# Kernel optimization log

Measured on AMD Instinct MI355X. Metric: run time of the kernel, lower is better.

The kernel has to match this reference:

```python
import jax, jax.numpy as jnp
import numpy as np

HIDDEN = 2048
N_HEADS = 32
N_KV = 8
HEAD_DIM = 128
EPS = 1e-6
THETA = 10000.0
WINDOW = 512
T = 2048


def _rms_norm(x, w, eps=EPS):
    # x: [..., d]
    var = jnp.mean(x * x, axis=-1, keepdims=True)
    return x * jax.lax.rsqrt(var + eps) * w


def _rope(x, positions):
    # neox-style full rotary, x: [T, H, d]
    d = x.shape[-1]
    inv_freq = 1.0 / (THETA ** (jnp.arange(0, d, 2, dtype=jnp.float32) / d))  # [d/2]
    ang = positions.astype(jnp.float32)[:, None] * inv_freq  # [T, d/2]
    cos = jnp.cos(ang)[:, None, :]  # [T,1,d/2]
    sin = jnp.sin(ang)[:, None, :]
    x1, x2 = x[..., : d // 2], x[..., d // 2 :]
    return jnp.concatenate([x1 * cos - x2 * sin, x2 * cos + x1 * sin], axis=-1)


def setup_inputs() -> dict:
    key = jax.random.key(0)
    ks = jax.random.split(key, 6)
    q_size = N_HEADS * HEAD_DIM
    kv_size = N_KV * HEAD_DIM
    s = 1.0 / np.sqrt(HIDDEN)
    return {
        "positions": jnp.arange(T, dtype=jnp.int32),
        "hidden_states": jax.random.normal(ks[0], (T, HIDDEN), dtype=jnp.float32),
        "w_qkv": jax.random.normal(ks[1], (HIDDEN, q_size + 2 * kv_size), dtype=jnp.float32) * s,
        "w_o": jax.random.normal(ks[2], (q_size, HIDDEN), dtype=jnp.float32) * s,
        "w_g": jax.random.normal(ks[3], (HIDDEN, N_HEADS), dtype=jnp.float32) * s,
        "q_norm_w": jnp.ones((HEAD_DIM,), dtype=jnp.float32),
        "k_norm_w": jnp.ones((HEAD_DIM,), dtype=jnp.float32),
    }


def reference(positions, hidden_states, w_qkv, w_o, w_g, q_norm_w, k_norm_w):
    t = hidden_states.shape[0]
    q_size = N_HEADS * HEAD_DIM
    kv_size = N_KV * HEAD_DIM
    scale = HEAD_DIM ** -0.5
    group = N_HEADS // N_KV

    qkv = hidden_states @ w_qkv  # [T, q+2kv]
    q = qkv[:, :q_size].reshape(t, N_HEADS, HEAD_DIM)
    k = qkv[:, q_size : q_size + kv_size].reshape(t, N_KV, HEAD_DIM)
    v = qkv[:, q_size + kv_size :].reshape(t, N_KV, HEAD_DIM)

    # per-head RMSNorm then RoPE
    q = _rope(_rms_norm(q, q_norm_w), positions)
    k = _rope(_rms_norm(k, k_norm_w), positions)

    # sliding-window causal attention with GQA (group queries per kv head)
    qg = q.reshape(t, N_KV, group, HEAD_DIM)
    scores = jnp.einsum("tkgd,skd->kgts", qg, k) * scale  # [Hkv,G,T,T]
    diff = positions[:, None] - positions[None, :]  # i - j
    mask = (diff >= 0) & (diff < WINDOW)  # causal + sliding window
    scores = jnp.where(mask[None, None], scores, -jnp.inf)
    probs = jax.nn.softmax(scores, axis=-1)
    attn = jnp.einsum("kgts,skd->tkgd", probs, v).reshape(t, N_HEADS, HEAD_DIM)

    # softplus gate per head, then output projection
    gate = jax.nn.softplus((hidden_states @ w_g).astype(jnp.float32)).astype(attn.dtype)
    attn = attn * gate[:, :, None]
    return attn.reshape(t, q_size) @ w_o
```

## Files before the change

### kernel.cpp

```cpp
#include <hip/hip_runtime.h>

typedef __attribute__((ext_vector_type(4))) float floatx4;
typedef __attribute__((ext_vector_type(8))) _Float16 half8;
typedef __attribute__((ext_vector_type(4))) _Float16 half4;

#define TT 2048
#define HIDDEN 2048
#define NH 32
#define NKV 8
#define HD 128
#define QSIZE 4096
#define KVSIZE 1024
#define QKVN 6144
#define QKVNP 6272
#define VOFF 5120
#define GOFF 6144
#define WINDOW 512

__global__ __launch_bounds__(256) void prep_kernel(
    const float* __restrict__ w_qkv, const float* __restrict__ w_o,
    const float* __restrict__ hidden, _Float16* __restrict__ Wqkvt,
    _Float16* __restrict__ Wot, _Float16* __restrict__ Xb) {
  __shared__ float tile[64][68];
  int bid = blockIdx.x;
  int tid = threadIdx.x;
  if (bid >= 5120) {
    if (bid < 7168) {
      int i = ((bid - 5120) * 256 + tid) * 8;
      float4 a = *(const float4*)&hidden[i];
      float4 b = *(const float4*)&hidden[i + 4];
      alignas(16) _Float16 o[8] = {(_Float16)a.x, (_Float16)a.y, (_Float16)a.z, (_Float16)a.w,
                                   (_Float16)b.x, (_Float16)b.y, (_Float16)b.z, (_Float16)b.w};
      *(uint4*)&Xb[i] = *(const uint4*)o;
    } else {
      int i = ((bid - 7168) * 256 + tid) * 8;
      *(uint4*)&Wqkvt[(size_t)(GOFF + NH) * HIDDEN + i] = (uint4){0, 0, 0, 0};
    }
    return;
  }
  const float* in;
  _Float16* out;
  int R, C, tilesX, t;
  if (bid < 3072) { in = w_qkv; out = Wqkvt; R = HIDDEN; C = QKVN; tilesX = 96; t = bid; }
  else           { in = w_o;   out = Wot;   R = QSIZE;  C = HIDDEN; tilesX = 32; t = bid - 3072; }
  int bc = (t % tilesX) * 64, br = (t / tilesX) * 64;
  int rr = tid >> 4, l16 = tid & 15;
#pragma unroll
  for (int it = 0; it < 4; ++it) {
    int r = rr + it * 16;
    *(float4*)&tile[r][l16 * 4] = *(const float4*)&in[(size_t)(br + r) * C + bc + l16 * 4];
  }
  __syncthreads();
  int orow = tid >> 2, rr0 = (tid & 3) * 16;
  alignas(16) _Float16 tmp[16];
#pragma unroll
  for (int jj = 0; jj < 16; ++jj) tmp[jj] = (_Float16)tile[rr0 + jj][orow];
  *(uint4*)&out[(size_t)(bc + orow) * R + br + rr0] = *(const uint4*)&tmp[0];
  *(uint4*)&out[(size_t)(bc + orow) * R + br + rr0 + 8] = *(const uint4*)&tmp[8];
}

__global__ __launch_bounds__(256) void transpose_f32_f16_kernel(
    const float* __restrict__ in, _Float16* __restrict__ out, int R, int C) {
  __shared__ float tile[32][33];
  int bc = blockIdx.x * 32;
  int br = blockIdx.y * 32;
  int c = threadIdx.x & 31;
  int r0 = threadIdx.x >> 5;
#pragma unroll
  for (int i = 0; i < 4; ++i) {
    int r = r0 + 8 * i;
    tile[r][c] = in[(size_t)(br + r) * C + bc + c];
  }
  __syncthreads();
#pragma unroll
  for (int i = 0; i < 4; ++i) {
    int r = r0 + 8 * i;
    out[(size_t)(bc + r) * R + br + c] = (_Float16)tile[c][r];
  }
}

__global__ __launch_bounds__(256) void repack_kv_kernel(const _Float16* __restrict__ Kh,
                                                        const _Float16* __restrict__ QKVh,
                                                        _Float16* __restrict__ Kf,
                                                        _Float16* __restrict__ Vf) {
  __shared__ _Float16 tile[64][136];
  int st = blockIdx.x, kh = blockIdx.y;
  int s0 = st * 64;
  if (blockIdx.z == 0) {
    _Float16* dst = Kf + (size_t)(kh * 32 + st) * 8192;
#pragma unroll
    for (int i = 0; i < 4; ++i) {
      int c = threadIdx.x + i * 256;
      int jt = c >> 8, kc = (c >> 6) & 3, quad = (c >> 4) & 3, n16 = c & 15;
      uint4 v = *(const uint4*)&Kh[((size_t)(s0 + jt * 16 + n16) * NKV + kh) * HD +
                                   kc * 32 + quad * 8];
      *(uint4*)&dst[c * 8] = v;
    }
  } else {
#pragma unroll
    for (int i = 0; i < 4; ++i) {
      int c = threadIdx.x + i * 256;
      int row = c >> 4, part = c & 15;
      *(uint4*)&tile[row][part * 8] =
          *(const uint4*)&QKVh[(size_t)(s0 + row) * QKVNP + VOFF + kh * HD + part * 8];
    }
    __syncthreads();
    _Float16* dst = Vf + (size_t)(kh * 32 + st) * 8192;
#pragma unroll
    for (int i = 0; i < 4; ++i) {
      int c = threadIdx.x + i * 256;
      int jd = c >> 7, kc = (c >> 6) & 1, quad = (c >> 4) & 3, n16 = c & 15;
      int d = jd * 16 + n16, sb = kc * 32 + quad * 8;
      alignas(16) _Float16 tmp[8];
#pragma unroll
      for (int j = 0; j < 8; ++j) tmp[j] = tile[sb + j][d];
      *(uint4*)&dst[c * 8] = *(const uint4*)tmp;
    }
  }
}

__device__ __forceinline__ void async16(const _Float16* g, _Float16* l) {
  __builtin_amdgcn_global_load_lds((const __attribute__((address_space(1))) void*)g,
                                   (__attribute__((address_space(3))) void*)l, 16, 0, 0);
}

__device__ __forceinline__ void swizzle_mn(int& m0, int& n0) {
  int ntiles = gridDim.y;
  int pid = blockIdx.x + blockIdx.y * gridDim.x;
  int band = pid / (8 * ntiles);
  int wi = pid - band * (8 * ntiles);
  m0 = (band * 8 + (wi & 7)) * 128;
  n0 = (wi >> 3) * 128;
}

template <typename OutT>
__global__ __launch_bounds__(256, 2) void gemm_bt_kernel(
    const _Float16* __restrict__ A, const _Float16* __restrict__ Bt,
    OutT* __restrict__ C, int M, int N, int K) {
  __shared__ _Float16 As[128 * 64];
  __shared__ _Float16 Bs[128 * 64];
  int tid = threadIdx.x;
  int wave = tid >> 6, lane = tid & 63;
  int wm = wave >> 1, wn = wave & 1;
  int m0, n0;
  swizzle_mn(m0, n0);
  int lr = lane & 15;
  int quad = lane >> 4;
  floatx4 acc[4][4];
#pragma unroll
  for (int i = 0; i < 4; ++i)
#pragma unroll
    for (int j = 0; j < 4; ++j) acc[i][j] = (floatx4){0.f, 0.f, 0.f, 0.f};

  for (int k0 = 0; k0 < K; k0 += 64) {
    __syncthreads();
#pragma unroll
    for (int it = 0; it < 4; ++it) {
      int c = tid + it * 256;
      int row = c >> 3, j = c & 7;
      int jj = j ^ (row & 7);
      _Float16* la = &As[it * 2048 + wave * 512];
      _Float16* lb = &Bs[it * 2048 + wave * 512];
      async16(&A[(size_t)(m0 + row) * K + k0 + jj * 8], la);
      async16(&Bt[(size_t)(n0 + row) * K + k0 + jj * 8], lb);
    }
    __syncthreads();
#pragma unroll
    for (int kc = 0; kc < 2; ++kc) {
      int ch = kc * 4 + quad;
      half8 a[4], b[4];
#pragma unroll
      for (int i = 0; i < 4; ++i) {
        int r = wm * 64 + i * 16 + lr;
        a[i] = *(const half8*)&As[r * 64 + (ch ^ (r & 7)) * 8];
      }
#pragma unroll
      for (int j = 0; j < 4; ++j) {
        int r = wn * 64 + j * 16 + lr;
        b[j] = *(const half8*)&Bs[r * 64 + (ch ^ (r & 7)) * 8];
      }
#pragma unroll
      for (int i = 0; i < 4; ++i)
#pragma unroll
        for (int j = 0; j < 4; ++j)
          acc[i][j] = __builtin_amdgcn_mfma_f32_16x16x32_f16(a[i], b[j], acc[i][j], 0, 0, 0);
    }
  }
  int rq = quad * 4;
#pragma unroll
  for (int i = 0; i < 4; ++i)
#pragma unroll
    for (int j = 0; j < 4; ++j)
#pragma unroll
      for (int r = 0; r < 4; ++r) {
        int row = m0 + wm * 64 + i * 16 + rq + r;
        int col = n0 + wn * 64 + j * 16 + lr;
        C[(size_t)row * N + col] = (OutT)acc[i][j][r];
      }
}

__global__ __launch_bounds__(256, 2) void gemm_bt_splitk_kernel(
    const _Float16* __restrict__ A, const _Float16* __restrict__ Bt,
    float* __restrict__ C, int M, int N, int K, int Ks) {
  __shared__ _Float16 As[128 * 64];
  __shared__ _Float16 Bs[128 * 64];
  int tid = threadIdx.x;
  int wave = tid >> 6, lane = tid & 63;
  int wm = wave >> 1, wn = wave & 1;
  int m0, n0;
  swizzle_mn(m0, n0);
  int kb = blockIdx.z * Ks;
  int lr = lane & 15;
  int quad = lane >> 4;
  floatx4 acc[4][4];
#pragma unroll
  for (int i = 0; i < 4; ++i)
#pragma unroll
    for (int j = 0; j < 4; ++j) acc[i][j] = (floatx4){0.f, 0.f, 0.f, 0.f};

  for (int k0 = kb; k0 < kb + Ks; k0 += 64) {
    __syncthreads();
#pragma unroll
    for (int it = 0; it < 4; ++it) {
      int c = tid + it * 256;
      int row = c >> 3, j = c & 7;
      int jj = j ^ (row & 7);
      _Float16* la = &As[it * 2048 + wave * 512];
      _Float16* lb = &Bs[it * 2048 + wave * 512];
      async16(&A[(size_t)(m0 + row) * K + k0 + jj * 8], la);
      async16(&Bt[(size_t)(n0 + row) * K + k0 + jj * 8], lb);
    }
    __syncthreads();
#pragma unroll
    for (int kc = 0; kc < 2; ++kc) {
      int ch = kc * 4 + quad;
      half8 a[4], b[4];
#pragma unroll
      for (int i = 0; i < 4; ++i) {
        int r = wm * 64 + i * 16 + lr;
        a[i] = *(const half8*)&As[r * 64 + (ch ^ (r & 7)) * 8];
      }
#pragma unroll
      for (int j = 0; j < 4; ++j) {
        int r = wn * 64 + j * 16 + lr;
        b[j] = *(const half8*)&Bs[r * 64 + (ch ^ (r & 7)) * 8];
      }
#pragma unroll
      for (int i = 0; i < 4; ++i)
#pragma unroll
        for (int j = 0; j < 4; ++j)
          acc[i][j] = __builtin_amdgcn_mfma_f32_16x16x32_f16(a[i], b[j], acc[i][j], 0, 0, 0);
    }
  }
  int rq = quad * 4;
#pragma unroll
  for (int i = 0; i < 4; ++i)
#pragma unroll
    for (int j = 0; j < 4; ++j)
#pragma unroll
      for (int r = 0; r < 4; ++r) {
        int row = m0 + wm * 64 + i * 16 + rq + r;
        int col = n0 + wn * 64 + j * 16 + lr;
        unsafeAtomicAdd(&C[(size_t)row * N + col], acc[i][j][r]);
      }
}

__global__ __launch_bounds__(256) void normrope_kernel(
    const _Float16* __restrict__ qkv, const float* __restrict__ qw,
    const float* __restrict__ kw, const int* __restrict__ positions,
    _Float16* __restrict__ qh, _Float16* __restrict__ khb) {
  int wid = blockIdx.x * 4 + (threadIdx.x >> 6);
  int lane = threadIdx.x & 63;
  int t, hh;
  const _Float16* src;
  _Float16* dst;
  const float* w;
  if (wid < TT * NH) {
    t = wid >> 5; hh = wid & 31;
    src = qkv + (size_t)t * QKVNP + hh * HD;
    dst = qh + ((size_t)t * NH + hh) * HD;
    w = qw;
  } else {
    int r = wid - TT * NH;
    t = r >> 3; hh = r & 7;
    src = qkv + (size_t)t * QKVNP + QSIZE + hh * HD;
    dst = khb + ((size_t)t * NKV + hh) * HD;
    w = kw;
  }
  float x1 = (float)src[lane];
  float x2 = (float)src[lane + 64];
  float ss = x1 * x1 + x2 * x2;
#pragma unroll
  for (int off = 1; off < 64; off <<= 1) ss += __shfl_xor(ss, off);
  float rr = rsqrtf(ss * (1.0f / 128.0f) + 1e-6f);
  float n1 = x1 * rr * w[lane];
  float n2 = x2 * rr * w[lane + 64];
  float pos = (float)positions[t];
  float invf = exp2f(-(float)lane * (13.287712379549449f / 64.0f));
  float ang = pos * invf;
  float sn, cs;
  sincosf(ang, &sn, &cs);
  dst[lane] = (_Float16)(n1 * cs - n2 * sn);
  dst[lane + 64] = (_Float16)(n2 * cs + n1 * sn);
}

#define PSTR 68
#define M0 8.0f
__global__ __launch_bounds__(256, 2) void attn_kernel(
    const _Float16* __restrict__ Qh, const _Float16* __restrict__ Kf,
    const _Float16* __restrict__ Vf, const _Float16* __restrict__ QKVh,
    _Float16* __restrict__ Og) {
  const float scale = 0.08838834764831845f;
  __shared__ _Float16 Ps[4][2 * 16 * PSTR];
  int tid = threadIdx.x;
  int wave = tid >> 6, lane = tid & 63;
  int n16 = lane & 15, quad = lane >> 4;
  int t0 = blockIdx.x * 32;
  int kh = blockIdx.y;
  int h = kh * 4 + wave;
  _Float16* ps = Ps[wave];

  half8 qf[2][4];
#pragma unroll
  for (int mt = 0; mt < 2; ++mt)
#pragma unroll
    for (int kc = 0; kc < 4; ++kc)
      qf[mt][kc] = *(const half8*)&Qh[((size_t)(t0 + mt * 16 + n16) * NH + h) * HD +
                                      kc * 32 + quad * 8];

  floatx4 O[2][8];
  float lp[2][4];
#pragma unroll
  for (int mt = 0; mt < 2; ++mt) {
#pragma unroll
    for (int jd = 0; jd < 8; ++jd) O[mt][jd] = (floatx4){0.f, 0.f, 0.f, 0.f};
#pragma unroll
    for (int r = 0; r < 4; ++r) lp[mt][r] = 0.f;
  }

  int lo = t0 - (WINDOW - 1);
  if (lo < 0) lo = 0;
  int st0 = lo >> 6;
  int st1 = (t0 + 31) >> 6;

  half8 kfr[4][4];
  {
    const _Float16* kb = Kf + (size_t)(kh * 32 + st0) * 8192;
#pragma unroll
    for (int jt = 0; jt < 4; ++jt)
#pragma unroll
      for (int kc = 0; kc < 4; ++kc)
        kfr[jt][kc] = *(const half8*)&kb[(jt * 4 + kc) * 512 + lane * 8];
  }

  for (int st = st0; st <= st1; ++st) {
    int s0 = st * 64;
    const _Float16* vb = Vf + (size_t)(kh * 32 + st) * 8192;
    floatx4 S[2][4];
#pragma unroll
    for (int mt = 0; mt < 2; ++mt)
#pragma unroll
      for (int jt = 0; jt < 4; ++jt) S[mt][jt] = (floatx4){0.f, 0.f, 0.f, 0.f};
#pragma unroll
    for (int jt = 0; jt < 4; ++jt)
#pragma unroll
      for (int kc = 0; kc < 4; ++kc)
#pragma unroll
        for (int mt = 0; mt < 2; ++mt)
          S[mt][jt] = __builtin_amdgcn_mfma_f32_16x16x32_f16(qf[mt][kc], kfr[jt][kc],
                                                             S[mt][jt], 0, 0, 0);
    if (st < st1) {
      const _Float16* kb = Kf + (size_t)(kh * 32 + st + 1) * 8192;
#pragma unroll
      for (int jt = 0; jt < 4; ++jt)
#pragma unroll
        for (int kc = 0; kc < 4; ++kc)
          kfr[jt][kc] = *(const half8*)&kb[(jt * 4 + kc) * 512 + lane * 8];
    }
    bool interior = (t0 >= s0 + 63) && (t0 + 31 - s0 < WINDOW);
    if (interior) {
#pragma unroll
      for (int mt = 0; mt < 2; ++mt)
#pragma unroll
        for (int r = 0; r < 4; ++r) {
          float rs = 0.f;
#pragma unroll
          for (int jt = 0; jt < 4; ++jt) {
            float p = __expf(__builtin_fmaf(S[mt][jt][r], scale, -M0));
            rs += p;
            ps[(mt * 16 + quad * 4 + r) * PSTR + jt * 16 + n16] = (_Float16)p;
          }
          lp[mt][r] += rs;
        }
    } else {
#pragma unroll
      for (int mt = 0; mt < 2; ++mt)
#pragma unroll
        for (int r = 0; r < 4; ++r) {
          int tq = t0 + mt * 16 + quad * 4 + r;
          float rs = 0.f;
#pragma unroll
          for (int jt = 0; jt < 4; ++jt) {
            int diff = tq - (s0 + jt * 16 + n16);
            bool ok = (diff >= 0) && (diff < WINDOW);
            float p = ok ? __expf(__builtin_fmaf(S[mt][jt][r], scale, -M0)) : 0.f;
            rs += p;
            ps[(mt * 16 + quad * 4 + r) * PSTR + jt * 16 + n16] = (_Float16)p;
          }
          lp[mt][r] += rs;
        }
    }
    half8 pf[2][2];
#pragma unroll
    for (int mt = 0; mt < 2; ++mt)
#pragma unroll
      for (int kc = 0; kc < 2; ++kc) {
        half4 lo4 = *(const half4*)&ps[(mt * 16 + n16) * PSTR + kc * 32 + quad * 8];
        half4 hi4 = *(const half4*)&ps[(mt * 16 + n16) * PSTR + kc * 32 + quad * 8 + 4];
        pf[mt][kc] = (half8){lo4[0], lo4[1], lo4[2], lo4[3], hi4[0], hi4[1], hi4[2], hi4[3]};
      }
#pragma unroll
    for (int jd = 0; jd < 8; ++jd) {
#pragma unroll
      for (int kc = 0; kc < 2; ++kc) {
        half8 vfr = *(const half8*)&vb[(jd * 2 + kc) * 512 + lane * 8];
#pragma unroll
        for (int mt = 0; mt < 2; ++mt)
          O[mt][jd] = __builtin_amdgcn_mfma_f32_16x16x32_f16(pf[mt][kc], vfr, O[mt][jd], 0, 0, 0);
      }
    }
  }
#pragma unroll
  for (int mt = 0; mt < 2; ++mt)
#pragma unroll
    for (int r = 0; r < 4; ++r) {
      float l = lp[mt][r];
#pragma unroll
      for (int off = 1; off < 16; off <<= 1) l += __shfl_xor(l, off);
      int t = t0 + mt * 16 + quad * 4 + r;
      float gl = (float)QKVh[(size_t)t * QKVNP + GOFF + h];
      float g = (gl > 0.f) ? gl + log1pf(__expf(-gl)) : log1pf(__expf(gl));
      float inv = g / l;
#pragma unroll
      for (int jd = 0; jd < 8; ++jd)
        Og[(size_t)t * QSIZE + h * HD + jd * 16 + n16] = (_Float16)(O[mt][jd][r] * inv);
    }
}

extern "C" void kernel_launch(void* const* d_in, const int* in_sizes, int n_in,
                              void* d_out, int out_size, void* d_ws, size_t ws_size,
                              hipStream_t stream) {
  const int* positions = (const int*)d_in[0];
  const float* hidden = (const float*)d_in[1];
  const float* w_qkv = (const float*)d_in[2];
  const float* w_o = (const float*)d_in[3];
  const float* w_g = (const float*)d_in[4];
  const float* q_norm_w = (const float*)d_in[5];
  const float* k_norm_w = (const float*)d_in[6];
  float* out = (float*)d_out;

  char* ws = (char*)d_ws;
  size_t off = 0;
  auto alloc = [&](size_t bytes) {
    void* p = ws + off;
    off += (bytes + 255) & ~(size_t)255;
    return p;
  };
  _Float16* Xb = (_Float16*)alloc((size_t)TT * HIDDEN * 2);
  _Float16* Wqkvt = (_Float16*)alloc((size_t)QKVNP * HIDDEN * 2);
  _Float16* Wot = (_Float16*)alloc((size_t)HIDDEN * QSIZE * 2);
  _Float16* QKVh = (_Float16*)alloc((size_t)TT * QKVNP * 2);
  _Float16* Qh = (_Float16*)alloc((size_t)TT * NH * HD * 2);
  _Float16* Kh = (_Float16*)alloc((size_t)TT * NKV * HD * 2);
  _Float16* Kf = (_Float16*)alloc((size_t)NKV * 32 * 8192 * 2);
  _Float16* Vf = (_Float16*)alloc((size_t)NKV * 32 * 8192 * 2);
  _Float16* Og = (_Float16*)alloc((size_t)TT * QSIZE * 2);

  hipMemsetAsync(d_out, 0, (size_t)out_size * 4, stream);

  prep_kernel<<<7264, 256, 0, stream>>>(w_qkv, w_o, hidden, Wqkvt, Wot, Xb);
  transpose_f32_f16_kernel<<<dim3(1, HIDDEN / 32), 256, 0, stream>>>(
      w_g, Wqkvt + (size_t)GOFF * HIDDEN, HIDDEN, NH);
  gemm_bt_kernel<_Float16><<<dim3(TT / 128, QKVNP / 128), 256, 0, stream>>>(
      Xb, Wqkvt, QKVh, TT, QKVNP, HIDDEN);
  normrope_kernel<<<(TT * (NH + NKV)) / 4, 256, 0, stream>>>(QKVh, q_norm_w, k_norm_w,
                                                             positions, Qh, Kh);
  repack_kv_kernel<<<dim3(32, NKV, 2), 256, 0, stream>>>(Kh, QKVh, Kf, Vf);
  attn_kernel<<<dim3(TT / 32, NKV), 256, 0, stream>>>(Qh, Kf, Vf, QKVh, Og);
  gemm_bt_splitk_kernel<<<dim3(TT / 128, HIDDEN / 128, 2), 256, 0, stream>>>(
      Og, Wot, out, TT, HIDDEN, QSIZE, QSIZE / 2);
}
```

Baseline: 366.7 us.

## Halve attention query tile, fold w_g transpose into prep, raise split-K to four

The attention kernel now handles 16 queries per block instead of 32, which doubles the grid and cuts registers per wave, at the cost of loading each K/V tile for fewer queries. The separate w_g transpose launch is merged into prep_kernel as extra blocks, saving one kernel launch. The output projection's split-K goes from 2 to 4 for more parallelism, which adds more atomic accumulation traffic into the output.

```diff
diff --git a/kernel.cpp b/kernel.cpp
--- a/kernel.cpp
+++ b/kernel.cpp
@@ -19,8 +19,9 @@
 
 __global__ __launch_bounds__(256) void prep_kernel(
     const float* __restrict__ w_qkv, const float* __restrict__ w_o,
-    const float* __restrict__ hidden, _Float16* __restrict__ Wqkvt,
-    _Float16* __restrict__ Wot, _Float16* __restrict__ Xb) {
+    const float* __restrict__ hidden, const float* __restrict__ w_g,
+    _Float16* __restrict__ Wqkvt, _Float16* __restrict__ Wot,
+    _Float16* __restrict__ Xb) {
   __shared__ float tile[64][68];
   int bid = blockIdx.x;
   int tid = threadIdx.x;
@@ -32,9 +33,24 @@
       alignas(16) _Float16 o[8] = {(_Float16)a.x, (_Float16)a.y, (_Float16)a.z, (_Float16)a.w,
                                    (_Float16)b.x, (_Float16)b.y, (_Float16)b.z, (_Float16)b.w};
       *(uint4*)&Xb[i] = *(const uint4*)o;
-    } else {
+    } else if (bid < 7264) {
       int i = ((bid - 7168) * 256 + tid) * 8;
       *(uint4*)&Wqkvt[(size_t)(GOFF + NH) * HIDDEN + i] = (uint4){0, 0, 0, 0};
+    } else {
+      int br = (bid - 7264) * 32;
+      int c = tid & 31, r0 = tid >> 5;
+      __shared__ float gt[32][33];
+#pragma unroll
+      for (int i = 0; i < 4; ++i) {
+        int r = r0 + 8 * i;
+        gt[r][c] = w_g[(size_t)(br + r) * NH + c];
+      }
+      __syncthreads();
+#pragma unroll
+      for (int i = 0; i < 4; ++i) {
+        int r = r0 + 8 * i;
+        Wqkvt[(size_t)(GOFF + r) * HIDDEN + br + c] = (_Float16)gt[c][r];
+      }
     }
     return;
   }
@@ -57,26 +73,6 @@
   for (int jj = 0; jj < 16; ++jj) tmp[jj] = (_Float16)tile[rr0 + jj][orow];
   *(uint4*)&out[(size_t)(bc + orow) * R + br + rr0] = *(const uint4*)&tmp[0];
   *(uint4*)&out[(size_t)(bc + orow) * R + br + rr0 + 8] = *(const uint4*)&tmp[8];
-}
-
-__global__ __launch_bounds__(256) void transpose_f32_f16_kernel(
-    const float* __restrict__ in, _Float16* __restrict__ out, int R, int C) {
-  __shared__ float tile[32][33];
-  int bc = blockIdx.x * 32;
-  int br = blockIdx.y * 32;
-  int c = threadIdx.x & 31;
-  int r0 = threadIdx.x >> 5;
-#pragma unroll
-  for (int i = 0; i < 4; ++i) {
-    int r = r0 + 8 * i;
-    tile[r][c] = in[(size_t)(br + r) * C + bc + c];
-  }
-  __syncthreads();
-#pragma unroll
-  for (int i = 0; i < 4; ++i) {
-    int r = r0 + 8 * i;
-    out[(size_t)(bc + r) * R + br + c] = (_Float16)tile[c][r];
-  }
 }
 
 __global__ __launch_bounds__(256) void repack_kv_kernel(const _Float16* __restrict__ Kh,
@@ -311,37 +307,31 @@
     const _Float16* __restrict__ Vf, const _Float16* __restrict__ QKVh,
     _Float16* __restrict__ Og) {
   const float scale = 0.08838834764831845f;
-  __shared__ _Float16 Ps[4][2 * 16 * PSTR];
+  __shared__ _Float16 Ps[4][16 * PSTR];
   int tid = threadIdx.x;
   int wave = tid >> 6, lane = tid & 63;
   int n16 = lane & 15, quad = lane >> 4;
-  int t0 = blockIdx.x * 32;
+  int t0 = blockIdx.x * 16;
   int kh = blockIdx.y;
   int h = kh * 4 + wave;
   _Float16* ps = Ps[wave];
 
-  half8 qf[2][4];
-#pragma unroll
-  for (int mt = 0; mt < 2; ++mt)
-#pragma unroll
-    for (int kc = 0; kc < 4; ++kc)
-      qf[mt][kc] = *(const half8*)&Qh[((size_t)(t0 + mt * 16 + n16) * NH + h) * HD +
-                                      kc * 32 + quad * 8];
-
-  floatx4 O[2][8];
-  float lp[2][4];
-#pragma unroll
-  for (int mt = 0; mt < 2; ++mt) {
-#pragma unroll
-    for (int jd = 0; jd < 8; ++jd) O[mt][jd] = (floatx4){0.f, 0.f, 0.f, 0.f};
-#pragma unroll
-    for (int r = 0; r < 4; ++r) lp[mt][r] = 0.f;
-  }
+  half8 qf[4];
+#pragma unroll
+  for (int kc = 0; kc < 4; ++kc)
+    qf[kc] = *(const half8*)&Qh[((size_t)(t0 + n16) * NH + h) * HD + kc * 32 + quad * 8];
+
+  floatx4 O[8];
+  float lp[4];
+#pragma unroll
+  for (int jd = 0; jd < 8; ++jd) O[jd] = (floatx4){0.f, 0.f, 0.f, 0.f};
+#pragma unroll
+  for (int r = 0; r < 4; ++r) lp[r] = 0.f;
 
   int lo = t0 - (WINDOW - 1);
   if (lo < 0) lo = 0;
   int st0 = lo >> 6;
-  int st1 = (t0 + 31) >> 6;
+  int st1 = t0 >> 6;
 
   half8 kfr[4][4];
   {
@@ -356,19 +346,14 @@
   for (int st = st0; st <= st1; ++st) {
     int s0 = st * 64;
     const _Float16* vb = Vf + (size_t)(kh * 32 + st) * 8192;
-    floatx4 S[2][4];
-#pragma unroll
-    for (int mt = 0; mt < 2; ++mt)
-#pragma unroll
-      for (int jt = 0; jt < 4; ++jt) S[mt][jt] = (floatx4){0.f, 0.f, 0.f, 0.f};
+    floatx4 S[4];
+#pragma unroll
+    for (int jt = 0; jt < 4; ++jt) S[jt] = (floatx4){0.f, 0.f, 0.f, 0.f};
 #pragma unroll
     for (int jt = 0; jt < 4; ++jt)
 #pragma unroll
       for (int kc = 0; kc < 4; ++kc)
-#pragma unroll
-        for (int mt = 0; mt < 2; ++mt)
-          S[mt][jt] = __builtin_amdgcn_mfma_f32_16x16x32_f16(qf[mt][kc], kfr[jt][kc],
-                                                             S[mt][jt], 0, 0, 0);
+        S[jt] = __builtin_amdgcn_mfma_f32_16x16x32_f16(qf[kc], kfr[jt][kc], S[jt], 0, 0, 0);
     if (st < st1) {
       const _Float16* kb = Kf + (size_t)(kh * 32 + st + 1) * 8192;
 #pragma unroll
@@ -377,74 +362,64 @@
         for (int kc = 0; kc < 4; ++kc)
           kfr[jt][kc] = *(const half8*)&kb[(jt * 4 + kc) * 512 + lane * 8];
     }
-    bool interior = (t0 >= s0 + 63) && (t0 + 31 - s0 < WINDOW);
+    bool interior = (t0 >= s0 + 63) && (t0 + 15 - s0 < WINDOW);
     if (interior) {
 #pragma unroll
-      for (int mt = 0; mt < 2; ++mt)
-#pragma unroll
-        for (int r = 0; r < 4; ++r) {
-          float rs = 0.f;
-#pragma unroll
-          for (int jt = 0; jt < 4; ++jt) {
-            float p = __expf(__builtin_fmaf(S[mt][jt][r], scale, -M0));
-            rs += p;
-            ps[(mt * 16 + quad * 4 + r) * PSTR + jt * 16 + n16] = (_Float16)p;
-          }
-          lp[mt][r] += rs;
+      for (int r = 0; r < 4; ++r) {
+        float rs = 0.f;
+#pragma unroll
+        for (int jt = 0; jt < 4; ++jt) {
+          float p = __expf(__builtin_fmaf(S[jt][r], scale, -M0));
+          rs += p;
+          ps[(quad * 4 + r) * PSTR + jt * 16 + n16] = (_Float16)p;
         }
+        lp[r] += rs;
+      }
     } else {
 #pragma unroll
-      for (int mt = 0; mt < 2; ++mt)
-#pragma unroll
-        for (int r = 0; r < 4; ++r) {
-          int tq = t0 + mt * 16 + quad * 4 + r;
-          float rs = 0.f;
-#pragma unroll
-          for (int jt = 0; jt < 4; ++jt) {
-            int diff = tq - (s0 + jt * 16 + n16);
-            bool ok = (diff >= 0) && (diff < WINDOW);
-            float p = ok ? __expf(__builtin_fmaf(S[mt][jt][r], scale, -M0)) : 0.f;
-            rs += p;
-            ps[(mt * 16 + quad * 4 + r) * PSTR + jt * 16 + n16] = (_Float16)p;
-          }
-          lp[mt][r] += rs;
+      for (int r = 0; r < 4; ++r) {
+        int tq = t0 + quad * 4 + r;
+        float rs = 0.f;
+#pragma unroll
+        for (int jt = 0; jt < 4; ++jt) {
+          int diff = tq - (s0 + jt * 16 + n16);
+          bool ok = (diff >= 0) && (diff < WINDOW);
+          float p = ok ? __expf(__builtin_fmaf(S[jt][r], scale, -M0)) : 0.f;
+          rs += p;
+          ps[(quad * 4 + r) * PSTR + jt * 16 + n16] = (_Float16)p;
         }
-    }
-    half8 pf[2][2];
-#pragma unroll
-    for (int mt = 0; mt < 2; ++mt)
-#pragma unroll
-      for (int kc = 0; kc < 2; ++kc) {
-        half4 lo4 = *(const half4*)&ps[(mt * 16 + n16) * PSTR + kc * 32 + quad * 8];
-        half4 hi4 = *(const half4*)&ps[(mt * 16 + n16) * PSTR + kc * 32 + quad * 8 + 4];
-        pf[mt][kc] = (half8){lo4[0], lo4[1], lo4[2], lo4[3], hi4[0], hi4[1], hi4[2], hi4[3]};
-      }
+        lp[r] += rs;
+      }
+    }
+    half8 pf[2];
+#pragma unroll
+    for (int kc = 0; kc < 2; ++kc) {
+      half4 lo4 = *(const half4*)&ps[n16 * PSTR + kc * 32 + quad * 8];
+      half4 hi4 = *(const half4*)&ps[n16 * PSTR + kc * 32 + quad * 8 + 4];
+      pf[kc] = (half8){lo4[0], lo4[1], lo4[2], lo4[3], hi4[0], hi4[1], hi4[2], hi4[3]};
+    }
 #pragma unroll
     for (int jd = 0; jd < 8; ++jd) {
 #pragma unroll
       for (int kc = 0; kc < 2; ++kc) {
         half8 vfr = *(const half8*)&vb[(jd * 2 + kc) * 512 + lane * 8];
-#pragma unroll
-        for (int mt = 0; mt < 2; ++mt)
-          O[mt][jd] = __builtin_amdgcn_mfma_f32_16x16x32_f16(pf[mt][kc], vfr, O[mt][jd], 0, 0, 0);
-      }
-    }
-  }
-#pragma unroll
-  for (int mt = 0; mt < 2; ++mt)
-#pragma unroll
-    for (int r = 0; r < 4; ++r) {
-      float l = lp[mt][r];
-#pragma unroll
-      for (int off = 1; off < 16; off <<= 1) l += __shfl_xor(l, off);
-      int t = t0 + mt * 16 + quad * 4 + r;
-      float gl = (float)QKVh[(size_t)t * QKVNP + GOFF + h];
-      float g = (gl > 0.f) ? gl + log1pf(__expf(-gl)) : log1pf(__expf(gl));
-      float inv = g / l;
-#pragma unroll
-      for (int jd = 0; jd < 8; ++jd)
-        Og[(size_t)t * QSIZE + h * HD + jd * 16 + n16] = (_Float16)(O[mt][jd][r] * inv);
-    }
+        O[jd] = __builtin_amdgcn_mfma_f32_16x16x32_f16(pf[kc], vfr, O[jd], 0, 0, 0);
+      }
+    }
+  }
+#pragma unroll
+  for (int r = 0; r < 4; ++r) {
+    float l = lp[r];
+#pragma unroll
+    for (int off = 1; off < 16; off <<= 1) l += __shfl_xor(l, off);
+    int t = t0 + quad * 4 + r;
+    float gl = (float)QKVh[(size_t)t * QKVNP + GOFF + h];
+    float g = (gl > 0.f) ? gl + log1pf(__expf(-gl)) : log1pf(__expf(gl));
+    float inv = g / l;
+#pragma unroll
+    for (int jd = 0; jd < 8; ++jd)
+      Og[(size_t)t * QSIZE + h * HD + jd * 16 + n16] = (_Float16)(O[jd][r] * inv);
+  }
 }
 
 extern "C" void kernel_launch(void* const* d_in, const int* in_sizes, int n_in,
@@ -478,15 +453,13 @@
 
   hipMemsetAsync(d_out, 0, (size_t)out_size * 4, stream);
 
-  prep_kernel<<<7264, 256, 0, stream>>>(w_qkv, w_o, hidden, Wqkvt, Wot, Xb);
-  transpose_f32_f16_kernel<<<dim3(1, HIDDEN / 32), 256, 0, stream>>>(
-      w_g, Wqkvt + (size_t)GOFF * HIDDEN, HIDDEN, NH);
+  prep_kernel<<<7328, 256, 0, stream>>>(w_qkv, w_o, hidden, w_g, Wqkvt, Wot, Xb);
   gemm_bt_kernel<_Float16><<<dim3(TT / 128, QKVNP / 128), 256, 0, stream>>>(
       Xb, Wqkvt, QKVh, TT, QKVNP, HIDDEN);
   normrope_kernel<<<(TT * (NH + NKV)) / 4, 256, 0, stream>>>(QKVh, q_norm_w, k_norm_w,
                                                              positions, Qh, Kh);
   repack_kv_kernel<<<dim3(32, NKV, 2), 256, 0, stream>>>(Kh, QKVh, Kf, Vf);
-  attn_kernel<<<dim3(TT / 32, NKV), 256, 0, stream>>>(Qh, Kf, Vf, QKVh, Og);
-  gemm_bt_splitk_kernel<<<dim3(TT / 128, HIDDEN / 128, 2), 256, 0, stream>>>(
-      Og, Wot, out, TT, HIDDEN, QSIZE, QSIZE / 2);
-}
+  attn_kernel<<<dim3(TT / 16, NKV), 256, 0, stream>>>(Qh, Kf, Vf, QKVh, Og);
+  gemm_bt_splitk_kernel<<<dim3(TT / 128, HIDDEN / 128, 4), 256, 0, stream>>>(
+      Og, Wot, out, TT, HIDDEN, QSIZE, QSIZE / 4);
+}
```

Result: faster. 351.6 us (-4.1%).
